# Performance work log

Hardware: AMD Instinct MI355X
Metric: run time of the kernel (lower is better)

The kernel has to match this reference:

```python
import jax, jax.numpy as jnp
import numpy as np

N = 100000   # nodes
E = 800000   # directed edges (dst sorted)
D = 64       # input_dim
H = 64       # hidden_dim (must equal input_dim per fusion_layer shape)
L = 16       # latent_dim


def _lin(k, fan_in, fan_out):
    # torch nn.Linear-like init scale
    bound = 1.0 / np.sqrt(fan_in)
    kw, kb = jax.random.split(k)
    W = jax.random.uniform(kw, (fan_in, fan_out), jnp.float32, -bound, bound)
    b = jax.random.uniform(kb, (fan_out,), jnp.float32, -bound, bound)
    return W, b


def setup_inputs() -> dict:
    key = jax.random.key(0)
    ks = jax.random.split(key, 12)
    x = jax.random.normal(ks[0], (N, D), jnp.float32)
    edge_src = jax.random.randint(ks[1], (E,), 0, N, jnp.int32)
    edge_dst = jnp.sort(jax.random.randint(ks[2], (E,), 0, N, jnp.int32))
    eps = jax.random.normal(ks[3], (N, L), jnp.float32)
    W_agg, b_agg = _lin(ks[4], D, H)          # neighbor_aggregator
    W_fus, b_fus = _lin(ks[5], 2 * H, H)      # fusion_layer
    W1, b1 = _lin(ks[6], H, H)                # fc1 (input_dim==hidden_dim)
    W21, b21 = _lin(ks[7], H, L)              # fc21 -> mu
    W22, b22 = _lin(ks[8], H, L)              # fc22 -> logvar
    W3, b3 = _lin(ks[9], L, H)                # fc3
    W4, b4 = _lin(ks[10], H, D)               # fc4
    return {"x": x, "edge_src": edge_src, "edge_dst": edge_dst, "eps": eps,
            "W_agg": W_agg, "b_agg": b_agg, "W_fus": W_fus, "b_fus": b_fus,
            "W1": W1, "b1": b1, "W21": W21, "b21": b21,
            "W22": W22, "b22": b22, "W3": W3, "b3": b3, "W4": W4, "b4": b4}


def reference(x, edge_src, edge_dst, eps, W_agg, b_agg, W_fus, b_fus,
              W1, b1, W21, b21, W22, b22, W3, b3, W4, b4):
    n = x.shape[0]
    # aggregate_neighbors: segment-mean over variable-length neighbor lists;
    # nodes with no neighbors get zeros (sum==0, count clamped to 1).
    nsum = jax.ops.segment_sum(x[edge_src], edge_dst, num_segments=n)
    cnt = jax.ops.segment_sum(jnp.ones((edge_dst.shape[0],), x.dtype), edge_dst, num_segments=n)
    neighbor_avg = nsum / jnp.maximum(cnt, 1.0)[:, None]          # [N, D]
    neighbor_encoded = jax.nn.relu(neighbor_avg @ W_agg + b_agg)   # [N, H]
    combined = jnp.concatenate([x, neighbor_encoded], axis=1)      # [N, 2H]
    xf = jax.nn.relu(combined @ W_fus + b_fus)                     # [N, H]
    # VAE encode
    h1 = jax.nn.relu(xf @ W1 + b1)
    mu = h1 @ W21 + b21
    logvar = h1 @ W22 + b22
    # reparameterize (fixed eps for determinism)
    z = mu + eps * jnp.exp(0.5 * logvar)
    # decode
    h3 = jax.nn.relu(z @ W3 + b3)
    recon = jax.nn.sigmoid(h3 @ W4 + b4)
    return (recon, mu, logvar)
```

## Files before the change

### kernel.cpp

```cpp
#include <hip/hip_runtime.h>
#include <math.h>

#define N_NODES 100000
#define E_EDGES 800000
#define NT 16
#define NTILES (N_NODES / NT)
#define OFF_MU 6400000L
#define OFF_LV 8000000L

typedef __attribute__((ext_vector_type(8))) short short8;
typedef __attribute__((ext_vector_type(4))) float f32x4;
typedef __attribute__((ext_vector_type(4))) float float4v;

#define SW_AGG 0
#define SW_FUS 4096
#define SW_W1  12288
#define SW_W2  16384
#define SW_W3  18432
#define SW_W4  20480
#define SW_TOT 24576

#define PW_OFF (1 << 20)
#define XB_OFF (2 << 20)

#define PB_RS 3125
#define PB_W  7
#define PB_X  3125

__device__ __forceinline__ unsigned short f2bf(float f) {
    unsigned u = __float_as_uint(f);
    unsigned r = u + 0x7FFFu + ((u >> 16) & 1u);
    return (unsigned short)(r >> 16);
}
__device__ __forceinline__ float bf2f(unsigned short h) {
    return __uint_as_float(((unsigned)h) << 16);
}

__device__ __forceinline__ int pidx(int row, int col) {
    const int c = ((col >> 3) ^ (row & 7));
    return row * 64 + c * 8 + (col & 7);
}

__device__ void stage_w(const float* __restrict__ W, int Ksrc, int NC,
                        int NKT, int NJT_local, int jt_off,
                        int rb, short* sw, int tid) {
    const int tot = NJT_local * NKT * 64;
    for (int s = tid; s < tot; s += 256) {
        int f = s >> 6, l = s & 63;
        int jtl = f / NKT, kt = f - jtl * NKT;
        int col = jtl * 16 + (l & 15);
        int k0 = kt * 32 + ((l >> 4) << 3);
        short8 hi;
        #pragma unroll
        for (int i = 0; i < 8; ++i) {
            float v = (k0 + i < Ksrc) ? W[(k0 + i) * NC + col] : 0.0f;
            hi[i] = (short)f2bf(v);
        }
        int fg = (jt_off + jtl) * NKT + kt;
        *(short8*)&sw[rb + fg * 512 + l * 8] = hi;
    }
}

__global__ __launch_bounds__(256) void prep(
    const int* __restrict__ edge_dst, int* __restrict__ row_start,
    const float* __restrict__ W_agg, const float* __restrict__ W_fus,
    const float* __restrict__ W1,  const float* __restrict__ W21,
    const float* __restrict__ W22, const float* __restrict__ W3,
    const float* __restrict__ W4, short* __restrict__ gw,
    const float* __restrict__ x, short* __restrict__ xbf)
{
    const int b = blockIdx.x;
    const int tid = threadIdx.x;
    if (b < PB_RS) {
        const int e = b * 256 + tid;
        if (e >= E_EDGES) return;
        int d = edge_dst[e];
        int dprev = (e == 0) ? -1 : edge_dst[e - 1];
        for (int n = dprev + 1; n <= d; ++n) row_start[n] = e;
        if (e == E_EDGES - 1) {
            for (int n = d + 1; n <= N_NODES; ++n) row_start[n] = E_EDGES;
        }
    } else if (b < PB_RS + PB_W) {
        switch (b - PB_RS) {
            case 0: stage_w(W_agg, 64, 64, 2, 4, 0, SW_AGG, gw, tid); break;
            case 1: stage_w(W_fus, 128, 64, 4, 4, 0, SW_FUS, gw, tid); break;
            case 2: stage_w(W1,   64, 64, 2, 4, 0, SW_W1,  gw, tid); break;
            case 3: stage_w(W21,  64, 16, 2, 1, 0, SW_W2,  gw, tid); break;
            case 4: stage_w(W22,  64, 16, 2, 1, 1, SW_W2,  gw, tid); break;
            case 5: stage_w(W3,   16, 64, 1, 4, 0, SW_W3,  gw, tid); break;
            case 6: stage_w(W4,   64, 64, 2, 4, 0, SW_W4,  gw, tid); break;
        }
    } else {
        const int i = (b - PB_RS - PB_W) * 256 + tid;
        if (i >= N_NODES * 8) return;
        const float4v a = ((const float4v*)x)[i * 2];
        const float4v c = ((const float4v*)x)[i * 2 + 1];
        short8 s;
        s[0] = (short)f2bf(a.x); s[1] = (short)f2bf(a.y);
        s[2] = (short)f2bf(a.z); s[3] = (short)f2bf(a.w);
        s[4] = (short)f2bf(c.x); s[5] = (short)f2bf(c.y);
        s[6] = (short)f2bf(c.z); s[7] = (short)f2bf(c.w);
        ((short8*)xbf)[i] = s;
    }
}

__device__ __forceinline__ void frags_from_xbf(const short* __restrict__ xbf,
                                               long base, int lane, short8* h) {
    const int row = lane & 15, ko = (lane >> 4) * 8;
    const short* r = xbf + (base + row) * 64;
    h[0] = *(const short8*)&r[ko];
    h[1] = *(const short8*)&r[32 + ko];
}

template<int NKT>
__device__ __forceinline__ void frags_from_planes(const short* phi, int lane,
                                                  short8* hi) {
    const int row = lane & 15;
    #pragma unroll
    for (int kt = 0; kt < NKT; ++kt) {
        const int c = kt * 4 + (lane >> 4);
        const int idx = row * 64 + ((c ^ (row & 7)) << 3);
        hi[kt] = *(const short8*)&phi[idx];
    }
}

template<int NKT>
__device__ __forceinline__ f32x4 gemm_one(const short8* ah,
                                          const short* __restrict__ sw, int rb,
                                          int jt, float bias, int lane) {
    f32x4 acc = { bias, bias, bias, bias };
    #pragma unroll
    for (int kt = 0; kt < NKT; ++kt) {
        const short8 bhi = *(const short8*)&sw[rb + (jt * NKT + kt) * 512 + lane * 8];
        acc = __builtin_amdgcn_mfma_f32_16x16x32_bf16(ah[kt], bhi, acc, 0, 0, 0);
    }
    return acc;
}

__device__ __forceinline__ void write_slab_plane(short* phi, f32x4 c, int jt,
                                                 int lane, bool relu) {
    const int g = lane >> 4, cj = lane & 15;
    const int col = jt * 16 + cj;
    #pragma unroll
    for (int r = 0; r < 4; ++r) {
        float f = relu ? fmaxf(c[r], 0.0f) : c[r];
        phi[pidx(g * 4 + r, col)] = (short)f2bf(f);
    }
}

__device__ __forceinline__ float tree16(const float* v) {
    float a0 = (v[0] + v[1]) + (v[2] + v[3]);
    float a1 = (v[4] + v[5]) + (v[6] + v[7]);
    float a2 = (v[8] + v[9]) + (v[10] + v[11]);
    float a3 = (v[12] + v[13]) + (v[14] + v[15]);
    return (a0 + a1) + (a2 + a3);
}
__device__ __forceinline__ float tree8(const float* v) {
    return ((v[0] + v[1]) + (v[2] + v[3])) + ((v[4] + v[5]) + (v[6] + v[7]));
}

__global__ __launch_bounds__(256, 8) void vae_top(
    const short* __restrict__ xbf,
    const int* __restrict__ edge_src,
    const float* __restrict__ eps,
    const float* __restrict__ b_agg, const float* __restrict__ b_fus,
    const float* __restrict__ b1,  const float* __restrict__ b21,
    const float* __restrict__ b22, const float* __restrict__ b3,
    const float* __restrict__ b4,
    const short* __restrict__ gw,
    const int* __restrict__ row_start,
    float* __restrict__ out)
{
    __shared__ __align__(16) short sA[1024];
    __shared__ __align__(16) short sB[1024];

    const int tid  = threadIdx.x;
    const int lane = tid & 63;
    const int wid  = tid >> 6;
    const long base = (long)blockIdx.x * NT;
    const int cj = lane & 15, g = lane >> 4;

    const float bja = b_agg[wid * 16 + cj];
    const float bjf = b_fus[wid * 16 + cj];
    const float bj1 = b1[wid * 16 + cj];
    const float bj3 = b3[wid * 16 + cj];
    const float bj4 = b4[wid * 16 + cj];

    const unsigned short* xbu = (const unsigned short*)xbf;

    {
        const int rsv = row_start[(int)base + (lane < 17 ? lane : 16)];
        const int W0 = __builtin_amdgcn_readlane(rsv, wid * 4);
        int p0 = W0 + lane;      p0 = p0 < E_EDGES ? p0 : E_EDGES - 1;
        int p1 = W0 + 64 + lane; p1 = p1 < E_EDGES ? p1 : E_EDGES - 1;
        const int iv0 = edge_src[p0];
        const int iv1 = edge_src[p1];

        #pragma unroll
        for (int q = 0; q < 4; ++q) {
            const int node = wid * 4 + q;
            const int e0 = __builtin_amdgcn_readlane(rsv, node);
            const int e1 = __builtin_amdgcn_readlane(rsv, node + 1);
            const int deg = e1 - e0;
            const int te0 = e0 - W0;
            float sum;
            if (deg <= 8 && te0 + 7 < 128) {
                float v[8];
                #pragma unroll
                for (int i = 0; i < 8; ++i) {
                    const int te = te0 + i;
                    const int vsel = (te & 64) ? iv1 : iv0;
                    int ix = __builtin_amdgcn_readlane(vsel, te & 63);
                    const bool live = i < deg;
                    ix = live ? ix : 0;
                    float tv = bf2f(xbu[(long)ix * 64 + lane]);
                    v[i] = live ? tv : 0.0f;
                }
                sum = tree8(v);
            } else if (te0 + 15 < 128) {
                float v[16];
                #pragma unroll
                for (int i = 0; i < 16; ++i) {
                    const int te = te0 + i;
                    const int vsel = (te & 64) ? iv1 : iv0;
                    int ix = __builtin_amdgcn_readlane(vsel, te & 63);
                    const bool live = i < deg;
                    ix = live ? ix : 0;
                    float tv = bf2f(xbu[(long)ix * 64 + lane]);
                    v[i] = live ? tv : 0.0f;
                }
                sum = tree16(v);
                for (int e = e0 + 16; e < e1; ++e)
                    sum += bf2f(xbu[(long)edge_src[e] * 64 + lane]);
            } else {
                float v[16];
                #pragma unroll
                for (int i = 0; i < 16; ++i) {
                    const int ee = e0 + i;
                    const bool live = ee < e1;
                    const int ec = ee < E_EDGES ? ee : E_EDGES - 1;
                    int ix = edge_src[ec];
                    ix = live ? ix : 0;
                    float tv = bf2f(xbu[(long)ix * 64 + lane]);
                    v[i] = live ? tv : 0.0f;
                }
                sum = tree16(v);
                for (int e = e0 + 16; e < e1; ++e)
                    sum += bf2f(xbu[(long)edge_src[e] * 64 + lane]);
            }
            const float avg = sum / fmaxf((float)deg, 1.0f);
            sA[pidx(node, lane)] = (short)f2bf(avg);
        }
    }
    __syncthreads();

    short8 ah[4];
    f32x4 c;

    frags_from_planes<2>(sA, lane, ah);
    c = gemm_one<2>(ah, gw, SW_AGG, wid, bja, lane);
    write_slab_plane(sB, c, wid, lane, true);
    __syncthreads();

    frags_from_xbf(xbf, base, lane, ah);
    frags_from_planes<2>(sB, lane, ah + 2);
    c = gemm_one<4>(ah, gw, SW_FUS, wid, bjf, lane);
    write_slab_plane(sA, c, wid, lane, true);
    __syncthreads();

    frags_from_planes<2>(sA, lane, ah);
    c = gemm_one<2>(ah, gw, SW_W1, wid, bj1, lane);
    write_slab_plane(sB, c, wid, lane, true);
    __syncthreads();

    if (wid == 0) {
        frags_from_planes<2>(sB, lane, ah);
        const f32x4 cmu = gemm_one<2>(ah, gw, SW_W2, 0, b21[cj], lane);
        const f32x4 clv = gemm_one<2>(ah, gw, SW_W2, 1, b22[cj], lane);
        #pragma unroll
        for (int r = 0; r < 4; ++r) {
            const long node = base + g * 4 + r;
            out[OFF_MU + node * 16 + cj] = cmu[r];
            out[OFF_LV + node * 16 + cj] = clv[r];
            const float z = cmu[r] + eps[node * 16 + cj] * __expf(0.5f * clv[r]);
            sA[pidx(g * 4 + r, cj)] = (short)f2bf(z);
        }
    }
    __syncthreads();

    {
        short8 zh = {0,0,0,0,0,0,0,0};
        if (lane < 32) {
            const int row = lane & 15;
            const int cch = (lane >> 4);
            zh = *(const short8*)&sA[row * 64 + ((cch ^ (row & 7)) << 3)];
        }
        c = gemm_one<1>(&zh, gw, SW_W3, wid, bj3, lane);
    }
    write_slab_plane(sB, c, wid, lane, true);
    __syncthreads();

    frags_from_planes<2>(sB, lane, ah);
    c = gemm_one<2>(ah, gw, SW_W4, wid, bj4, lane);
    #pragma unroll
    for (int r = 0; r < 4; ++r) {
        const float s = 1.0f / (1.0f + __expf(-c[r]));
        out[(base + g * 4 + r) * 64 + wid * 16 + cj] = s;
    }
}

extern "C" void kernel_launch(void* const* d_in, const int* in_sizes, int n_in,
                              void* d_out, int out_size, void* d_ws, size_t ws_size,
                              hipStream_t stream) {
    const float* x        = (const float*)d_in[0];
    const int*   edge_src = (const int*)  d_in[1];
    const int*   edge_dst = (const int*)  d_in[2];
    const float* eps      = (const float*)d_in[3];
    const float* W_agg    = (const float*)d_in[4];
    const float* b_agg    = (const float*)d_in[5];
    const float* W_fus    = (const float*)d_in[6];
    const float* b_fus    = (const float*)d_in[7];
    const float* W1       = (const float*)d_in[8];
    const float* b1       = (const float*)d_in[9];
    const float* W21      = (const float*)d_in[10];
    const float* b21      = (const float*)d_in[11];
    const float* W22      = (const float*)d_in[12];
    const float* b22      = (const float*)d_in[13];
    const float* W3       = (const float*)d_in[14];
    const float* b3       = (const float*)d_in[15];
    const float* W4       = (const float*)d_in[16];
    const float* b4       = (const float*)d_in[17];
    float* out = (float*)d_out;

    int*   row_start = (int*)d_ws;
    short* gw        = (short*)((char*)d_ws + PW_OFF);
    short* xbf       = (short*)((char*)d_ws + XB_OFF);

    prep<<<PB_RS + PB_W + PB_X, 256, 0, stream>>>(edge_dst, row_start,
                                                  W_agg, W_fus, W1, W21, W22, W3, W4,
                                                  gw, x, xbf);
    vae_top<<<NTILES, 256, 0, stream>>>(xbf, edge_src, eps,
                                        b_agg, b_fus, b1, b21, b22, b3, b4,
                                        gw, row_start, out);
}
```

Before: 58.10 us.

## Hoist x-half of fusion GEMM before aggregation and compute mu/logvar redundantly per wave

The x-dependent half of the fusion GEMM now runs at kernel start, before the neighbor aggregation, and its accumulator is carried into the later neighbor-half MFMAs. This overlaps its loads and MFMAs with the gather latency. Every wave now computes mu/logvar and z redundantly into a private LDS slab, so the block-wide barrier after the wave-0-only stage goes away. The cost is extra MFMA and exp work in waves 1-3, plus more registers and LDS, which could lower occupancy.

```diff
diff --git a/kernel.cpp b/kernel.cpp
--- a/kernel.cpp
+++ b/kernel.cpp
@@ -124,14 +124,13 @@
     }
 }
 
-template<int NKT>
-__device__ __forceinline__ f32x4 gemm_one(const short8* ah,
-                                          const short* __restrict__ sw, int rb,
-                                          int jt, float bias, int lane) {
-    f32x4 acc = { bias, bias, bias, bias };
+template<int N>
+__device__ __forceinline__ f32x4 gemm_frags(const short8* ah,
+                                            const short* __restrict__ sw, int rb,
+                                            int fg0, f32x4 acc, int lane) {
     #pragma unroll
-    for (int kt = 0; kt < NKT; ++kt) {
-        const short8 bhi = *(const short8*)&sw[rb + (jt * NKT + kt) * 512 + lane * 8];
+    for (int kt = 0; kt < N; ++kt) {
+        const short8 bhi = *(const short8*)&sw[rb + (fg0 + kt) * 512 + lane * 8];
         acc = __builtin_amdgcn_mfma_f32_16x16x32_bf16(ah[kt], bhi, acc, 0, 0, 0);
     }
     return acc;
@@ -173,6 +172,7 @@
 {
     __shared__ __align__(16) short sA[1024];
     __shared__ __align__(16) short sB[1024];
+    __shared__ __align__(16) short sZ[4 * 16 * 24];
 
     const int tid  = threadIdx.x;
     const int lane = tid & 63;
@@ -185,8 +185,19 @@
     const float bj1 = b1[wid * 16 + cj];
     const float bj3 = b3[wid * 16 + cj];
     const float bj4 = b4[wid * 16 + cj];
+    const float b21l = b21[cj];
+    const float b22l = b22[cj];
 
     const unsigned short* xbu = (const unsigned short*)xbf;
+    short* sZw = sZ + wid * (16 * 24);
+
+    f32x4 cxf;
+    {
+        short8 xh[2];
+        frags_from_xbf(xbf, base, lane, xh);
+        f32x4 a0 = { bjf, bjf, bjf, bjf };
+        cxf = gemm_frags<2>(xh, gw, SW_FUS, wid * 4, a0, lane);
+    }
 
     {
         const int rsv = row_start[(int)base + (lane < 17 ? lane : 16)];
@@ -254,54 +265,60 @@
     }
     __syncthreads();
 
-    short8 ah[4];
+    short8 ah[2];
     f32x4 c;
 
     frags_from_planes<2>(sA, lane, ah);
-    c = gemm_one<2>(ah, gw, SW_AGG, wid, bja, lane);
+    { f32x4 a0 = { bja, bja, bja, bja };
+      c = gemm_frags<2>(ah, gw, SW_AGG, wid * 2, a0, lane); }
     write_slab_plane(sB, c, wid, lane, true);
     __syncthreads();
 
-    frags_from_xbf(xbf, base, lane, ah);
-    frags_from_planes<2>(sB, lane, ah + 2);
-    c = gemm_one<4>(ah, gw, SW_FUS, wid, bjf, lane);
+    frags_from_planes<2>(sB, lane, ah);
+    c = gemm_frags<2>(ah, gw, SW_FUS, wid * 4 + 2, cxf, lane);
     write_slab_plane(sA, c, wid, lane, true);
     __syncthreads();
 
     frags_from_planes<2>(sA, lane, ah);
-    c = gemm_one<2>(ah, gw, SW_W1, wid, bj1, lane);
+    { f32x4 a0 = { bj1, bj1, bj1, bj1 };
+      c = gemm_frags<2>(ah, gw, SW_W1, wid * 2, a0, lane); }
     write_slab_plane(sB, c, wid, lane, true);
     __syncthreads();
 
-    if (wid == 0) {
+    {
         frags_from_planes<2>(sB, lane, ah);
-        const f32x4 cmu = gemm_one<2>(ah, gw, SW_W2, 0, b21[cj], lane);
-        const f32x4 clv = gemm_one<2>(ah, gw, SW_W2, 1, b22[cj], lane);
+        f32x4 amu = { b21l, b21l, b21l, b21l };
+        f32x4 alv = { b22l, b22l, b22l, b22l };
+        const f32x4 cmu = gemm_frags<2>(ah, gw, SW_W2, 0, amu, lane);
+        const f32x4 clv = gemm_frags<2>(ah, gw, SW_W2, 2, alv, lane);
         #pragma unroll
         for (int r = 0; r < 4; ++r) {
             const long node = base + g * 4 + r;
-            out[OFF_MU + node * 16 + cj] = cmu[r];
-            out[OFF_LV + node * 16 + cj] = clv[r];
+            if (wid == 0) {
+                out[OFF_MU + node * 16 + cj] = cmu[r];
+                out[OFF_LV + node * 16 + cj] = clv[r];
+            }
             const float z = cmu[r] + eps[node * 16 + cj] * __expf(0.5f * clv[r]);
-            sA[pidx(g * 4 + r, cj)] = (short)f2bf(z);
-        }
-    }
-    __syncthreads();
+            sZw[(g * 4 + r) * 24 + cj] = (short)f2bf(z);
+        }
+    }
 
     {
         short8 zh = {0,0,0,0,0,0,0,0};
         if (lane < 32) {
             const int row = lane & 15;
-            const int cch = (lane >> 4);
-            zh = *(const short8*)&sA[row * 64 + ((cch ^ (row & 7)) << 3)];
-        }
-        c = gemm_one<1>(&zh, gw, SW_W3, wid, bj3, lane);
-    }
-    write_slab_plane(sB, c, wid, lane, true);
-    __syncthreads();
-
-    frags_from_planes<2>(sB, lane, ah);
-    c = gemm_one<2>(ah, gw, SW_W4, wid, bj4, lane);
+            const int ch = lane >> 4;
+            zh = *(const short8*)&sZw[row * 24 + ch * 8];
+        }
+        f32x4 a0 = { bj3, bj3, bj3, bj3 };
+        c = gemm_frags<1>(&zh, gw, SW_W3, wid, a0, lane);
+    }
+    write_slab_plane(sA, c, wid, lane, true);
+    __syncthreads();
+
+    frags_from_planes<2>(sA, lane, ah);
+    { f32x4 a0 = { bj4, bj4, bj4, bj4 };
+      c = gemm_frags<2>(ah, gw, SW_W4, wid * 2, a0, lane); }
     #pragma unroll
     for (int r = 0; r < 4; ++r) {
         const float s = 1.0f / (1.0f + __expf(-c[r]));
```

Result: slower. 77.42 us (+33.2%).
